# Kernel optimization log

Measured on AMD Instinct MI355X. Metric: run time of the kernel, lower is better.

The kernel has to match this reference:

```python
import jax, jax.numpy as jnp
import numpy as np

N, E, G, B = 50000, 1600000, 128, 128
FP = 33     # num_feature_pro
ED = 128    # embed_dim
ML = 3000   # max_len


def setup_inputs() -> dict:
    key = jax.random.key(0)
    ks = jax.random.split(key, 20)
    s = lambda k, shape: jax.random.normal(k, shape, jnp.float32) * 0.02
    inp = {}
    inp["pro_x"] = jax.random.normal(ks[0], (N, FP), jnp.float32)
    inp["edge_index"] = jax.random.randint(ks[1], (2, E), 0, N)
    inp["edge_weight"] = jax.random.uniform(ks[2], (E,), jnp.float32)
    inp["pro_batch"] = jnp.sort(jax.random.randint(ks[3], (N,), 0, G))
    inp["rna_global"] = jax.random.randint(ks[4], (B, ML), 0, 5)
    inp["rna_local"] = jax.random.randint(ks[5], (B, ML - 2), 0, 65)
    inp["emb1"] = s(ks[6], (5, ED))
    inp["emb2"] = s(ks[7], (65, ED))
    inp["convW1"] = s(ks[8], (32, ML, 8));     inp["convb1"] = jnp.zeros((32,), jnp.float32)
    inp["convW2"] = s(ks[9], (32, ML - 2, 8)); inp["convb2"] = jnp.zeros((32,), jnp.float32)
    inp["fcxr_W"] = s(ks[10], (32 * 121, 128)); inp["fcxr_b"] = jnp.zeros((128,), jnp.float32)
    inp["gcn1_W"] = s(ks[11], (FP, FP));         inp["gcn1_b"] = jnp.zeros((FP,), jnp.float32)
    inp["gcn2_W"] = s(ks[12], (FP, 2 * FP));     inp["gcn2_b"] = jnp.zeros((2 * FP,), jnp.float32)
    inp["gcn3_W"] = s(ks[13], (2 * FP, 4 * FP)); inp["gcn3_b"] = jnp.zeros((4 * FP,), jnp.float32)
    inp["bn1_g"] = jnp.ones((FP,), jnp.float32);     inp["bn1_b"] = jnp.zeros((FP,), jnp.float32)
    inp["bn2_g"] = jnp.ones((2 * FP,), jnp.float32); inp["bn2_b"] = jnp.zeros((2 * FP,), jnp.float32)
    inp["bn3_g"] = jnp.ones((4 * FP,), jnp.float32); inp["bn3_b"] = jnp.zeros((4 * FP,), jnp.float32)
    inp["fcg1_W"] = s(ks[14], (4 * FP, 1024)); inp["fcg1_b"] = jnp.zeros((1024,), jnp.float32)
    inp["fcg2_W"] = s(ks[15], (1024, 128));    inp["fcg2_b"] = jnp.zeros((128,), jnp.float32)
    return inp


def _gcn(x, W, b, src, dst, ew, n):
    # PyG GCNConv: x' = D^{-1/2}(A+I)D^{-1/2} (x W) + b, self-loop weight 1
    xw = x @ W                                           # [n, out]
    deg = jax.ops.segment_sum(ew, dst, num_segments=n) + 1.0
    dis = jax.lax.rsqrt(deg)
    norm = dis[src] * ew * dis[dst]                      # [E]
    out = jax.ops.segment_sum(xw[src] * norm[:, None], dst, num_segments=n)
    out = out + xw * (dis * dis)[:, None]                # self loops
    return out + b


def _bn(x, g, b, eps=1e-5):
    # NodeLevelBatchNorm (training): batch stats over the node dim, biased var
    m = x.mean(0)
    v = ((x - m) ** 2).mean(0)
    return (x - m) * jax.lax.rsqrt(v + eps) * g + b


def _conv1d(x, W, b):
    # x: [B, C, L], W: [O, C, K] -> [B, O, L-K+1]
    y = jax.lax.conv_general_dilated(x, W, (1,), 'VALID',
                                     dimension_numbers=('NCH', 'OIH', 'NCH'))
    return y + b[None, :, None]


def _rna(tok, emb, cW, cb, fW, fb):
    e = emb[tok]                     # [B, seq, 128] -> channels=seq, length=128
    y = _conv1d(e, cW, cb)           # [B, 32, 121]
    return y.reshape(y.shape[0], -1) @ fW + fb


def reference(pro_x, edge_index, edge_weight, pro_batch, rna_global, rna_local,
              emb1, emb2, convW1, convb1, convW2, convb2, fcxr_W, fcxr_b,
              gcn1_W, gcn1_b, gcn2_W, gcn2_b, gcn3_W, gcn3_b,
              bn1_g, bn1_b, bn2_g, bn2_b, bn3_g, bn3_b,
              fcg1_W, fcg1_b, fcg2_W, fcg2_b):
    src, dst = edge_index[0], edge_index[1]
    n = pro_x.shape[0]
    # RNA branch (fc_xr shared between global and local)
    xrg = _rna(rna_global, emb1, convW1, convb1, fcxr_W, fcxr_b)
    xrl = _rna(rna_local, emb2, convW2, convb2, fcxr_W, fcxr_b)
    # Protein GCN branch
    xp = jax.nn.relu(_bn(_gcn(pro_x, gcn1_W, gcn1_b, src, dst, edge_weight, n), bn1_g, bn1_b))
    ones = jnp.ones_like(edge_weight)
    xp = jax.nn.relu(_bn(_gcn(xp, gcn2_W, gcn2_b, src, dst, ones, n), bn2_g, bn2_b))
    xp = jax.nn.relu(_bn(_gcn(xp, gcn3_W, gcn3_b, src, dst, ones, n), bn3_g, bn3_b))
    # global mean pool per graph
    cnt = jax.ops.segment_sum(jnp.ones((n,), xp.dtype), pro_batch, num_segments=G)
    pooled = jax.ops.segment_sum(xp, pro_batch, num_segments=G) / jnp.maximum(cnt, 1.0)[:, None]
    h = jax.nn.relu(pooled @ fcg1_W + fcg1_b)
    xp_out = h @ fcg2_W + fcg2_b     # dropout = identity (eval)
    xc_rna = (xrg + xrl) * 0.5       # mean over stacked [xrg, xrl]
    return (xc_rna, xp_out)
```

## Files before the change

kernel.cpp:

```cpp
#include <hip/hip_runtime.h>
#include <hip/hip_bf16.h>

typedef __hip_bfloat16 bf16;
typedef unsigned short u16;

#define NN 50000
#define NE 1600000
#define NG 128
#define NB 128
#define SG 3000
#define SL 2998
#define VG 5
#define VL 65
#define EDB 6250
#define AGB 12500
#define NA  (NB*VG + NB*VL)
#define NGB (32*VG + 32*VL)
#define CASTB ((NN*40+255)/256)
#define NSTR 8

__device__ __forceinline__ float b2f(bf16 x){ return __bfloat162float(x); }
__device__ __forceinline__ float blo(unsigned u){ return __uint_as_float(u << 16); }
__device__ __forceinline__ float bhi(unsigned u){ return __uint_as_float(u & 0xffff0000u); }

__global__ void k_front(const int* __restrict__ rna_g, const int* __restrict__ rna_l,
                        int* __restrict__ tcnt_g, int* __restrict__ toff_g,
                        u16* __restrict__ bucket_g,
                        int* __restrict__ tcnt_l, int* __restrict__ toff_l,
                        u16* __restrict__ bucket_l,
                        const float* __restrict__ convW1, const float* __restrict__ convW2,
                        float* __restrict__ Wr1, float* __restrict__ Wr2,
                        const float* __restrict__ fcxrW, const float* __restrict__ cb1,
                        const float* __restrict__ cb2, float* __restrict__ bias0,
                        const int* __restrict__ dst, const float* __restrict__ ew,
                        double* __restrict__ packed, int* __restrict__ slot){
    int bx = blockIdx.x;
    int t = threadIdx.x;
    if (bx < 2*NB){
        __shared__ int hist[VL], pre[VL], cur[VL];
        int br = bx & 1, b = bx >> 1;
        const int* tok = br ? rna_l : rna_g;
        int S = br ? SL : SG, V = br ? VL : VG;
        int* tcnt = br ? tcnt_l : tcnt_g;
        int* toff = br ? toff_l : toff_g;
        u16* bucket = br ? bucket_l : bucket_g;
        if (t < V) hist[t] = 0;
        __syncthreads();
        for (int i = t; i < S; i += 256) atomicAdd(&hist[tok[b*S + i]], 1);
        __syncthreads();
        if (t == 0){
            int run = 0;
            for (int v = 0; v < V; ++v){ pre[v] = run; run += hist[v]; }
        }
        __syncthreads();
        if (t < V){
            tcnt[b*V + t] = hist[t];
            toff[b*V + t] = pre[t];
            cur[t] = pre[t];
        }
        __syncthreads();
        for (int i = t; i < S; i += 256){
            int v = tok[b*S + i];
            int p = atomicAdd(&cur[v], 1);
            bucket[b*S + p] = (u16)i;
        }
        return;
    }
    bx -= 2*NB;
    if (bx < EDB){
        int e = bx*256 + t;
        double old = unsafeAtomicAdd(&packed[dst[e]], 1048576.0 + (double)ew[e]);
        slot[e] = (int)(old * (1.0/1048576.0));
        return;
    }
    bx -= EDB;
    if (bx < SG + SL){
        const float* W; float* Wr; int S, c = bx;
        if (c < SG){ W = convW1; Wr = Wr1; S = SG; }
        else { c -= SG; W = convW2; Wr = Wr2; S = SL; }
        Wr[c*256 + t] = W[((t >> 3)*S + c)*8 + (t & 7)];
        return;
    }
    bx -= SG + SL;
    if (t >= 128) return;
    int o = bx, j = t;
    float s = 0.f;
    const float* Wo = fcxrW + o*121*128 + j;
    for (int l = 0; l < 121; ++l) s += Wo[l*128];
    unsafeAtomicAdd(&bias0[j], 0.5f * (cb1[o] + cb2[o]) * s);
}

__device__ void dev_buildA(const float* __restrict__ Wr, const u16* __restrict__ bucket,
                           const int* __restrict__ toff, const int* __restrict__ tcnt,
                           float* __restrict__ A, int S, int V, int bv){
    int b = bv / V, v = bv - b*V;
    int t = threadIdx.x;
    const u16* bk = bucket + b*S + toff[b*V + v];
    int m = tcnt[b*V + v];
    float acc = 0.f;
    int idx = 0;
    for (; idx + 4 <= m; idx += 4){
        int c0 = bk[idx], c1 = bk[idx+1], c2 = bk[idx+2], c3 = bk[idx+3];
        acc += Wr[c0*256 + t];
        acc += Wr[c1*256 + t];
        acc += Wr[c2*256 + t];
        acc += Wr[c3*256 + t];
    }
    for (; idx < m; ++idx) acc += Wr[bk[idx]*256 + t];
    A[b*(256*V) + v*256 + t] = acc;
}

__global__ void k_F1(const float* __restrict__ Wr1, const float* __restrict__ Wr2,
                     const u16* __restrict__ bucket_g, const int* __restrict__ toff_g,
                     const int* __restrict__ tcnt_g, float* __restrict__ Ag,
                     const u16* __restrict__ bucket_l, const int* __restrict__ toff_l,
                     const int* __restrict__ tcnt_l, float* __restrict__ Al,
                     const double* __restrict__ packed, int* __restrict__ cnt,
                     float2* __restrict__ dis12, float2* __restrict__ self12,
                     const int* __restrict__ batch, int* __restrict__ gstart,
                     int* __restrict__ bsum,
                     const float* __restrict__ fcxrb, const float* __restrict__ bias0,
                     float* __restrict__ out0){
    __shared__ int sd[256];
    int bx = blockIdx.x;
    if (bx < NA){
        if (bx < NB*VG) dev_buildA(Wr1, bucket_g, toff_g, tcnt_g, Ag, SG, VG, bx);
        else dev_buildA(Wr2, bucket_l, toff_l, tcnt_l, Al, SL, VL, bx - NB*VG);
        return;
    }
    bx -= NA;
    int t = threadIdx.x;
    if (bx == 49){
        for (int idx = t; idx < NB*128; idx += 256)
            out0[idx] = fcxrb[idx & 127] + bias0[idx & 127];
        return;
    }
    int base = bx*1024;
    int s = 0;
    #pragma unroll
    for (int j = 0; j < 4; ++j){
        int i = base + t*4 + j;
        if (i < NN){
            double p = packed[i];
            int c = (int)(p * (1.0/1048576.0));
            float w = (float)(p - (double)c * 1048576.0);
            cnt[i] = c; s += c;
            float r1 = rsqrtf(w + 1.0f);
            float r2 = rsqrtf((float)c + 1.0f);
            dis12[i] = make_float2(r1, r2);
            self12[i] = make_float2(r1*r1, r2*r2);
            int pb = batch[i];
            int prev = (i == 0) ? -1 : batch[i-1];
            for (int g = prev + 1; g <= pb; ++g) gstart[g] = i;
            if (i == NN - 1){
                for (int g = pb + 1; g <= NG; ++g) gstart[g] = NN;
            }
        }
    }
    sd[t] = s; __syncthreads();
    for (int d = 128; d > 0; d >>= 1){
        if (t < d) sd[t] += sd[t+d];
        __syncthreads();
    }
    if (t == 0) bsum[bx] = sd[0];
}

__global__ void k_scan3(const int* __restrict__ cnt, const int* __restrict__ bsum,
                        int* __restrict__ offs){
    __shared__ int sd[256];
    __shared__ int sbase;
    int t = threadIdx.x;
    if (t == 0){
        int run = 0;
        for (int i = 0; i < blockIdx.x; ++i) run += bsum[i];
        sbase = run;
    }
    int base = blockIdx.x*1024;
    int loc[4]; int s = 0;
    #pragma unroll
    for (int j = 0; j < 4; ++j){
        int idx = base + t*4 + j;
        loc[j] = (idx < NN) ? cnt[idx] : 0;
        s += loc[j];
    }
    sd[t] = s; __syncthreads();
    for (int d = 1; d < 256; d <<= 1){
        int v = (t >= d) ? sd[t-d] : 0;
        __syncthreads();
        sd[t] += v;
        __syncthreads();
    }
    int run = sbase + (sd[t] - s);
    #pragma unroll
    for (int j = 0; j < 4; ++j){
        int idx = base + t*4 + j;
        if (idx < NN) offs[idx] = run;
        run += loc[j];
    }
}

__device__ void dev_buildG(float (*rows)[128], const float* __restrict__ emb,
                           const float* __restrict__ W, bf16* __restrict__ G,
                           int V, int q){
    int o = q / V, mt = q - o*V;
    int t = threadIdx.x;
    int j = t & 127, half = t >> 7;
    int kk[4], vv[4];
    #pragma unroll
    for (int qq = 0; qq < 4; ++qq){
        int mm = half*4 + qq;
        int m = mt*8 + mm;
        int k = m / V, v = m - k*V;
        kk[qq] = k; vv[qq] = v;
        rows[mm][j] = emb[v*128 + j];
    }
    __syncthreads();
    float a0=0.f, a1=0.f, a2=0.f, a3=0.f;
    const float* Wo = W + o*121*128 + j;
    for (int l = 0; l < 121; ++l){
        float w = Wo[l*128];
        a0 += rows[half*4+0][l + kk[0]] * w;
        a1 += rows[half*4+1][l + kk[1]] * w;
        a2 += rows[half*4+2][l + kk[2]] * w;
        a3 += rows[half*4+3][l + kk[3]] * w;
    }
    float a[4] = {a0, a1, a2, a3};
    #pragma unroll
    for (int qq = 0; qq < 4; ++qq){
        int row = vv[qq]*256 + o*8 + kk[qq];
        G[(size_t)row*128 + j] = __float2bfloat16(a[qq]);
    }
}

__global__ void k_F2(const int* __restrict__ src, const int* __restrict__ dst,
                     const float* __restrict__ ew, const float2* __restrict__ dis12,
                     const int* __restrict__ offs, const int* __restrict__ slot,
                     float4* __restrict__ epk,
                     const float* __restrict__ emb1, const float* __restrict__ emb2,
                     const float* __restrict__ fcxrW, bf16* __restrict__ G1,
                     bf16* __restrict__ G2,
                     const float* __restrict__ pro_x, bf16* __restrict__ xb0){
    __shared__ float rows[8][128];
    int bx = blockIdx.x;
    if (bx < 32*VG){ dev_buildG(rows, emb1, fcxrW, G1, VG, bx); return; }
    if (bx < NGB){ dev_buildG(rows, emb2, fcxrW, G2, VL, bx - 32*VG); return; }
    bx -= NGB;
    if (bx < EDB){
        int e = bx*256 + threadIdx.x;
        int s = src[e], d = dst[e];
        int pos = offs[d] + slot[e];
        float2 a = dis12[s], b = dis12[d];
        float4 v;
        v.x = __int_as_float(s*80);
        v.y = a.x * ew[e] * b.x;
        v.z = a.y * b.y;
        v.w = __int_as_float(s*144);
        epk[pos] = v;
        return;
    }
    bx -= EDB;
    int i = bx*256 + threadIdx.x;
    if (i >= NN*40) return;
    int n = i / 40, f = i - n*40;
    xb0[i] = __float2bfloat16(f < 33 ? pro_x[n*33 + f] : 0.f);
}

template<int QV, int GRP, int OFF_W, int N_Z>
__device__ void dev_agg(float* sAgg ,
                        const bf16* __restrict__ xb, const float4* __restrict__ epk,
                        const int* __restrict__ offs, const int* __restrict__ cnt,
                        const float2* __restrict__ self12,
                        const float* __restrict__ W, const float* __restrict__ bias,
                        float* __restrict__ tout, float* __restrict__ bnpart,
                        int F, int OF, int bx){
    const int LPG = 64 / GRP;
    int wave = threadIdx.x >> 6;
    int node = bx*4 + wave;
    int lane = threadIdx.x & 63;
    int grp  = lane / LPG;
    int gl   = lane % LPG;
    bool act = gl < QV;
    const char* xc = (const char*)xb;
    float a0=0,a1=0,a2=0,a3=0,a4=0,a5=0,a6=0,a7=0;
    int b = offs[node], e = b + cnt[node];
    if (act){
        int fo = gl << 4;
        if (grp == 0){
            float2 sw2 = self12[node];
            float sw = N_Z ? sw2.y : sw2.x;
            uint4 u = *(const uint4*)(xc + node*(QV*16) + fo);
            a0 = sw*blo(u.x); a1 = sw*bhi(u.x); a2 = sw*blo(u.y); a3 = sw*bhi(u.y);
            a4 = sw*blo(u.z); a5 = sw*bhi(u.z); a6 = sw*blo(u.w); a7 = sw*bhi(u.w);
        }
        int p = b + grp;
        for (; p + 3*GRP < e; p += 4*GRP){
            float4 e0 = epk[p];
            float4 e1 = epk[p +   GRP];
            float4 e2 = epk[p + 2*GRP];
            float4 e3 = epk[p + 3*GRP];
            int o0 = __float_as_int(OFF_W ? e0.w : e0.x); float n0 = N_Z ? e0.z : e0.y;
            int o1 = __float_as_int(OFF_W ? e1.w : e1.x); float n1 = N_Z ? e1.z : e1.y;
            int o2 = __float_as_int(OFF_W ? e2.w : e2.x); float n2 = N_Z ? e2.z : e2.y;
            int o3 = __float_as_int(OFF_W ? e3.w : e3.x); float n3 = N_Z ? e3.z : e3.y;
            uint4 u0 = *(const uint4*)(xc + o0 + fo);
            uint4 u1 = *(const uint4*)(xc + o1 + fo);
            uint4 u2 = *(const uint4*)(xc + o2 + fo);
            uint4 u3 = *(const uint4*)(xc + o3 + fo);
            a0 += n0*blo(u0.x); a1 += n0*bhi(u0.x); a2 += n0*blo(u0.y); a3 += n0*bhi(u0.y);
            a4 += n0*blo(u0.z); a5 += n0*bhi(u0.z); a6 += n0*blo(u0.w); a7 += n0*bhi(u0.w);
            a0 += n1*blo(u1.x); a1 += n1*bhi(u1.x); a2 += n1*blo(u1.y); a3 += n1*bhi(u1.y);
            a4 += n1*blo(u1.z); a5 += n1*bhi(u1.z); a6 += n1*blo(u1.w); a7 += n1*bhi(u1.w);
            a0 += n2*blo(u2.x); a1 += n2*bhi(u2.x); a2 += n2*blo(u2.y); a3 += n2*bhi(u2.y);
            a4 += n2*blo(u2.z); a5 += n2*bhi(u2.z); a6 += n2*blo(u2.w); a7 += n2*bhi(u2.w);
            a0 += n3*blo(u3.x); a1 += n3*bhi(u3.x); a2 += n3*blo(u3.y); a3 += n3*bhi(u3.y);
            a4 += n3*blo(u3.z); a5 += n3*bhi(u3.z); a6 += n3*blo(u3.w); a7 += n3*bhi(u3.w);
        }
        if (p < e){
            int p1 = p + GRP, p2 = p + 2*GRP;
            bool v1 = p1 < e, v2 = p2 < e;
            float4 e0 = epk[p];
            float4 e1 = epk[v1 ? p1 : p];
            float4 e2 = epk[v2 ? p2 : p];
            int o0 = __float_as_int(OFF_W ? e0.w : e0.x);
            int o1 = __float_as_int(OFF_W ? e1.w : e1.x);
            int o2 = __float_as_int(OFF_W ? e2.w : e2.x);
            float n0 = N_Z ? e0.z : e0.y;
            float n1 = v1 ? (N_Z ? e1.z : e1.y) : 0.f;
            float n2 = v2 ? (N_Z ? e2.z : e2.y) : 0.f;
            uint4 u0 = *(const uint4*)(xc + o0 + fo);
            uint4 u1 = *(const uint4*)(xc + o1 + fo);
            uint4 u2 = *(const uint4*)(xc + o2 + fo);
            a0 += n0*blo(u0.x); a1 += n0*bhi(u0.x); a2 += n0*blo(u0.y); a3 += n0*bhi(u0.y);
            a4 += n0*blo(u0.z); a5 += n0*bhi(u0.z); a6 += n0*blo(u0.w); a7 += n0*bhi(u0.w);
            a0 += n1*blo(u1.x); a1 += n1*bhi(u1.x); a2 += n1*blo(u1.y); a3 += n1*bhi(u1.y);
            a4 += n1*blo(u1.z); a5 += n1*bhi(u1.z); a6 += n1*blo(u1.w); a7 += n1*bhi(u1.w);
            a0 += n2*blo(u2.x); a1 += n2*bhi(u2.x); a2 += n2*blo(u2.y); a3 += n2*bhi(u2.y);
            a4 += n2*blo(u2.z); a5 += n2*bhi(u2.z); a6 += n2*blo(u2.w); a7 += n2*bhi(u2.w);
        }
    }
    #pragma unroll
    for (int m = LPG; m < 64; m <<= 1){
        a0 += __shfl_xor(a0, m); a1 += __shfl_xor(a1, m);
        a2 += __shfl_xor(a2, m); a3 += __shfl_xor(a3, m);
        a4 += __shfl_xor(a4, m); a5 += __shfl_xor(a5, m);
        a6 += __shfl_xor(a6, m); a7 += __shfl_xor(a7, m);
    }
    if (act && grp == 0){
        float4* dst = (float4*)&sAgg[wave*(QV*8) + gl*8];
        dst[0] = make_float4(a0, a1, a2, a3);
        dst[1] = make_float4(a4, a5, a6, a7);
    }
    __syncthreads();
    int i0 = bx*4;
    int j = threadIdx.x;
    if (j < OF){
        float c0 = bias[j], c1 = c0, c2 = c0, c3 = c0;
        const float* Wj = W + j;
        const float* s0 = sAgg;
        const float* s1 = sAgg + QV*8;
        const float* s2 = sAgg + 2*QV*8;
        const float* s3 = sAgg + 3*QV*8;
        #pragma unroll 4
        for (int f = 0; f < F; ++f){
            float w = Wj[f*OF];
            c0 += s0[f]*w; c1 += s1[f]*w; c2 += s2[f]*w; c3 += s3[f]*w;
        }
        tout[(size_t)(i0+0)*OF + j] = c0;
        tout[(size_t)(i0+1)*OF + j] = c1;
        tout[(size_t)(i0+2)*OF + j] = c2;
        tout[(size_t)(i0+3)*OF + j] = c3;
        float s  = c0 + c1 + c2 + c3;
        float ss = c0*c0 + c1*c1 + c2*c2 + c3*c3;
        float* part = bnpart + (bx & (NSTR-1))*(2*OF);
        unsafeAtomicAdd(&part[j], s);
        unsafeAtomicAdd(&part[OF + j], ss);
    }
}

template<int QV, int GRP, int OFF_W, int N_Z>
__global__ __launch_bounds__(256, 8)
void k_agg_gemm(const bf16* __restrict__ xb, const float4* __restrict__ epk,
                const int* __restrict__ offs, const int* __restrict__ cnt,
                const float2* __restrict__ self12,
                const float* __restrict__ W, const float* __restrict__ bias,
                float* __restrict__ tout, float* __restrict__ bnpart,
                int F, int OF){
    __shared__ float sAgg[4*QV*8];
    dev_agg<QV,GRP,OFF_W,N_Z>(sAgg, xb, epk, offs, cnt, self12, W, bias,
                              tout, bnpart, F, OF, blockIdx.x);
}

__device__ void dev_gemmR(float* xs , int bq,
                          const float* __restrict__ Ag, const bf16* __restrict__ G1,
                          const float* __restrict__ Al, const bf16* __restrict__ G2,
                          float* __restrict__ out0){
    int kpart = bq >> 4;
    int bgrp  = bq & 15;
    const float* X; const bf16* G; int K, k0;
    if (kpart < 5){ X = Ag; G = G1; K = 1280;  k0 = kpart*256; }
    else          { X = Al; G = G2; K = 16640; k0 = (kpart-5)*256; }
    int b0 = bgrp*8;
    int t = threadIdx.x;
    #pragma unroll
    for (int i = 0; i < 8; ++i)
        xs[i*256 + t] = X[(b0+i)*K + k0 + t];
    __syncthreads();
    int rq = t >> 7, j = t & 127;
    const float* x0 = xs + (rq*4)*256;
    float a0=0,a1=0,a2=0,a3=0;
    const bf16* Gp = G + (size_t)k0*128 + j;
    for (int kk = 0; kk < 256; ++kk){
        float g = b2f(Gp[kk*128]);
        a0 += x0[kk]*g; a1 += x0[256+kk]*g; a2 += x0[512+kk]*g; a3 += x0[768+kk]*g;
    }
    unsafeAtomicAdd(&out0[(b0+rq*4+0)*128 + j], 0.5f*a0);
    unsafeAtomicAdd(&out0[(b0+rq*4+1)*128 + j], 0.5f*a1);
    unsafeAtomicAdd(&out0[(b0+rq*4+2)*128 + j], 0.5f*a2);
    unsafeAtomicAdd(&out0[(b0+rq*4+3)*128 + j], 0.5f*a3);
}

__global__ void k_L3(const bf16* __restrict__ xb, const float4* __restrict__ epk,
                     const int* __restrict__ offs, const int* __restrict__ cnt,
                     const float2* __restrict__ self12,
                     const float* __restrict__ W, const float* __restrict__ bias,
                     float* __restrict__ tout, float* __restrict__ bnpart,
                     const float* __restrict__ Ag, const bf16* __restrict__ G1,
                     const float* __restrict__ Al, const bf16* __restrict__ G2,
                     float* __restrict__ out0){
    __shared__ float smem[8*256];
    int bx = blockIdx.x;
    if (bx < AGB){
        dev_agg<9,4,1,1>(smem, xb, epk, offs, cnt, self12, W, bias, tout, bnpart,
                         66, 132, bx);
    } else {
        dev_gemmR(smem, bx - AGB, Ag, G1, Al, G2, out0);
    }
}

__global__ void k_bn_apply(const float* __restrict__ t, const float* __restrict__ part,
                           const float* __restrict__ g, const float* __restrict__ b,
                           bf16* __restrict__ xo, int OF, int OS, int total){
    __shared__ float fs[264];
    int tid = threadIdx.x;
    for (int i = tid; i < 2*OF; i += 256){
        float s = 0.f;
        #pragma unroll
        for (int k = 0; k < NSTR; ++k) s += part[k*(2*OF) + i];
        fs[i] = s;
    }
    __syncthreads();
    int id = blockIdx.x*256 + tid;
    if (id >= total) return;
    int i = id / OS, f = id - i*OS;
    float v = 0.f;
    if (f < OF){
        float m  = fs[f] * (1.0f/(float)NN);
        float vr = fs[OF + f] * (1.0f/(float)NN) - m*m;
        float sc = g[f] * rsqrtf(vr + 1e-5f);
        float sh = b[f] - m*sc;
        v = t[(size_t)i*OF + f] * sc + sh;
        v = v > 0.f ? v : 0.f;
    }
    xo[id] = __float2bfloat16(v);
}

__global__ void k_fcgF(const float* __restrict__ bufB, const float* __restrict__ part3,
                       const float* __restrict__ bn3g, const float* __restrict__ bn3b,
                       const int* __restrict__ gstart,
                       const float* __restrict__ W1, const float* __restrict__ b1,
                       const float* __restrict__ W2, const float* __restrict__ b2,
                       float* __restrict__ out){
    __shared__ float fs[264];
    __shared__ float scs[132], shs[132];
    __shared__ float pp[7][132];
    __shared__ float pr[132];
    __shared__ float hr[1024];
    __shared__ float part[8][128];
    int g = blockIdx.x, t = threadIdx.x;
    for (int i = t; i < 264; i += 1024){
        float s = 0.f;
        #pragma unroll
        for (int k = 0; k < NSTR; ++k) s += part3[k*264 + i];
        fs[i] = s;
    }
    __syncthreads();
    if (t < 132){
        float m  = fs[t] * (1.0f/(float)NN);
        float vr = fs[132 + t] * (1.0f/(float)NN) - m*m;
        float sc = bn3g[t] * rsqrtf(vr + 1e-5f);
        scs[t] = sc;
        shs[t] = bn3b[t] - m*sc;
    }
    __syncthreads();
    int i0 = gstart[g], i1 = gstart[g+1];
    int r = t / 132, f = t - r*132;
    if (r < 7){
        float acc = 0.f;
        for (int i = i0 + r; i < i1; i += 7){
            float v = bufB[(size_t)i*132 + f] * scs[f] + shs[f];
            acc += v > 0.f ? v : 0.f;
        }
        pp[r][f] = acc;
    }
    __syncthreads();
    if (t < 132){
        float s = 0.f;
        #pragma unroll
        for (int k = 0; k < 7; ++k) s += pp[k][t];
        float inv = 1.0f / fmaxf((float)(i1 - i0), 1.0f);
        pr[t] = s * inv;
    }
    __syncthreads();
    float acc = b1[t];
    #pragma unroll 4
    for (int ff = 0; ff < 132; ++ff) acc += pr[ff] * W1[ff*1024 + t];
    hr[t] = acc > 0.f ? acc : 0.f;
    __syncthreads();
    int ks = t >> 7, j = t & 127;
    const float* Wp = W2 + (ks*128)*128 + j;
    const float* hp = hr + ks*128;
    float a = 0.f;
    #pragma unroll 8
    for (int kk = 0; kk < 128; ++kk) a += hp[kk] * Wp[(size_t)kk*128];
    part[ks][j] = a;
    __syncthreads();
    if (t < 128){
        float s = b2[t];
        #pragma unroll
        for (int rr = 0; rr < 8; ++rr) s += part[rr][t];
        out[g*128 + t] = s;
    }
}

extern "C" void kernel_launch(void* const* d_in, const int* in_sizes, int n_in,
                              void* d_out, int out_size, void* d_ws, size_t ws_size,
                              hipStream_t stream)
{
    (void)in_sizes; (void)n_in; (void)out_size; (void)ws_size;

    const float* pro_x  = (const float*)d_in[0];
    const int*   eidx   = (const int*)  d_in[1];
    const float* ew     = (const float*)d_in[2];
    const int*   pbatch = (const int*)  d_in[3];
    const int*   rna_g  = (const int*)  d_in[4];
    const int*   rna_l  = (const int*)  d_in[5];
    const float* emb1   = (const float*)d_in[6];
    const float* emb2   = (const float*)d_in[7];
    const float* convW1 = (const float*)d_in[8];
    const float* convb1 = (const float*)d_in[9];
    const float* convW2 = (const float*)d_in[10];
    const float* convb2 = (const float*)d_in[11];
    const float* fcxrW  = (const float*)d_in[12];
    const float* fcxrb  = (const float*)d_in[13];
    const float* g1W = (const float*)d_in[14];
    const float* g1b = (const float*)d_in[15];
    const float* g2W = (const float*)d_in[16];
    const float* g2b = (const float*)d_in[17];
    const float* g3W = (const float*)d_in[18];
    const float* g3b = (const float*)d_in[19];
    const float* bn1g = (const float*)d_in[20];
    const float* bn1b = (const float*)d_in[21];
    const float* bn2g = (const float*)d_in[22];
    const float* bn2b = (const float*)d_in[23];
    const float* bn3g = (const float*)d_in[24];
    const float* bn3b = (const float*)d_in[25];
    const float* fcg1W = (const float*)d_in[26];
    const float* fcg1b = (const float*)d_in[27];
    const float* fcg2W = (const float*)d_in[28];
    const float* fcg2b = (const float*)d_in[29];

    const int* e_src = eidx;
    const int* e_dst = eidx + NE;

    char* base = (char*)d_ws;
    size_t off = 0;
    auto alloc = [&](size_t bytes)->char*{
        off = (off + 255) & ~(size_t)255;
        char* p = base + off; off += bytes; return p;
    };

    double* packed  = (double*)alloc(NN*8);
    float* bias0   = (float*)alloc(128*4);
    float* bnpart1 = (float*)alloc(NSTR*2*33*4);
    float* bnpart2 = (float*)alloc(NSTR*2*66*4);
    float* bnpart3 = (float*)alloc(NSTR*2*132*4);
    size_t zero_bytes = (off + 255) & ~(size_t)255;

    int*    cnt    = (int*)   alloc(NN*4);
    float2* dis12  = (float2*)alloc(NN*8);
    float2* self12 = (float2*)alloc(NN*8);
    int*    offs   = (int*)   alloc(NN*4);
    int*    bsum   = (int*)   alloc(64*4);
    int*    gstart = (int*)   alloc((NG+1)*4);
    float4* epk    = (float4*)alloc((size_t)NE*16);
    float*  bufB   = (float*) alloc((size_t)NN*132*4);
    bf16*   xbA    = (bf16*)  alloc((size_t)NE*4);
    bf16*   xbB    = (bf16*)  alloc((size_t)NN*72*2);
    float*  Ag     = (float*) alloc((size_t)NB*256*VG*4);
    float*  Al     = (float*) alloc((size_t)NB*256*VL*4);
    bf16*   G1     = (bf16*)  alloc((size_t)32*8*VG*128*2);
    bf16*   G2     = (bf16*)  alloc((size_t)32*8*VL*128*2);

    int*  slot = (int*)xbA;
    bf16* xb0  = (bf16*)xbB;

    float* out0 = (float*)d_out;
    float* out1 = (float*)d_out + 16384;

    char* rb = (char*)bufB;
    size_t ro = 0;
    auto ralloc = [&](size_t bytes)->char*{
        ro = (ro + 255) & ~(size_t)255;
        char* p = rb + ro; ro += bytes; return p;
    };
    int* toff_g   = (int*)ralloc(NB*VG*4);
    int* toff_l   = (int*)ralloc(NB*VL*4);
    int* tcnt_g   = (int*)ralloc(NB*VG*4);
    int* tcnt_l   = (int*)ralloc(NB*VL*4);
    u16* bucket_g = (u16*)ralloc((size_t)NB*SG*2);
    u16* bucket_l = (u16*)ralloc((size_t)NB*SL*2);
    float* Wr1    = (float*)ralloc((size_t)SG*256*4);
    float* Wr2    = (float*)ralloc((size_t)SL*256*4);

    hipMemsetAsync(d_ws, 0, zero_bytes, stream);

    k_front<<<2*NB + EDB + SG + SL + 32, 256, 0, stream>>>(
        rna_g, rna_l, tcnt_g, toff_g, bucket_g, tcnt_l, toff_l, bucket_l,
        convW1, convW2, Wr1, Wr2, fcxrW, convb1, convb2, bias0,
        e_dst, ew, packed, slot);

    k_F1<<<NA + 50, 256, 0, stream>>>(Wr1, Wr2,
                                      bucket_g, toff_g, tcnt_g, Ag,
                                      bucket_l, toff_l, tcnt_l, Al,
                                      packed, cnt, dis12, self12, pbatch, gstart,
                                      bsum, fcxrb, bias0, out0);
    k_scan3<<<49, 256, 0, stream>>>(cnt, bsum, offs);

    k_F2<<<NGB + EDB + CASTB, 256, 0, stream>>>(
        e_src, e_dst, ew, dis12, offs, slot, epk,
        emb1, emb2, fcxrW, G1, G2, pro_x, xb0);

    k_agg_gemm<5,8,0,0><<<AGB, 256, 0, stream>>>(xb0, epk, offs, cnt, self12,
                                                 g1W, g1b, bufB, bnpart1, 33, 33);
    k_bn_apply<<<(NN*40+255)/256, 256, 0, stream>>>(bufB, bnpart1, bn1g, bn1b,
                                                    xbA, 33, 40, NN*40);

    k_agg_gemm<5,8,0,1><<<AGB, 256, 0, stream>>>(xbA, epk, offs, cnt, self12,
                                                 g2W, g2b, bufB, bnpart2, 33, 66);
    k_bn_apply<<<(NN*72+255)/256, 256, 0, stream>>>(bufB, bnpart2, bn2g, bn2b,
                                                    xbB, 66, 72, NN*72);

    k_L3<<<AGB + 1120, 256, 0, stream>>>(xbB, epk, offs, cnt, self12,
                                         g3W, g3b, bufB, bnpart3, Ag, G1, Al, G2, out0);

    k_fcgF<<<NG, 1024, 0, stream>>>(bufB, bnpart3, bn3g, bn3b, gstart,
                                    fcg1W, fcg1b, fcg2W, fcg2b, out1);
}
```

Measured before the change: 656.7 us.

## Spread BN atomics over 64 stripes, reduce them in a separate kernel, prefetch edges

Raises the number of striped partial-sum buffers for batch-norm statistics from 8 to 64 to cut atomic contention in the aggregation kernels. A new single-block kernel reduces the 64 stripes once into a sums buffer, so the apply and final kernels no longer redo the reduction in every block. It also software-pipelines the edge-record loads in the aggregation loop, fetching the next group of four while the current group is processed. The cost is three extra kernel launches, a larger zeroed workspace, and more live registers in the aggregation loop.

Result: faster. 580.6 us (-11.6%).

```diff
diff --git a/kernel.cpp b/kernel.cpp
--- a/kernel.cpp
+++ b/kernel.cpp
@@ -17,7 +17,6 @@
 #define NA  (NB*VG + NB*VL)
 #define NGB (32*VG + 32*VL)
 #define CASTB ((NN*40+255)/256)
-#define NSTR 8
 
 __device__ __forceinline__ float b2f(bf16 x){ return __bfloat162float(x); }
 __device__ __forceinline__ float blo(unsigned u){ return __uint_as_float(u << 16); }
@@ -283,6 +282,7 @@
     const char* xc = (const char*)xb;
     float a0=0,a1=0,a2=0,a3=0,a4=0,a5=0,a6=0,a7=0;
     int b = offs[node], e = b + cnt[node];
+    int p = b + grp;
     if (act){
         int fo = gl << 4;
         if (grp == 0){
@@ -292,28 +292,41 @@
             a0 = sw*blo(u.x); a1 = sw*bhi(u.x); a2 = sw*blo(u.y); a3 = sw*bhi(u.y);
             a4 = sw*blo(u.z); a5 = sw*bhi(u.z); a6 = sw*blo(u.w); a7 = sw*bhi(u.w);
         }
-        int p = b + grp;
-        for (; p + 3*GRP < e; p += 4*GRP){
+        if (p + 3*GRP < e){
             float4 e0 = epk[p];
             float4 e1 = epk[p +   GRP];
             float4 e2 = epk[p + 2*GRP];
             float4 e3 = epk[p + 3*GRP];
-            int o0 = __float_as_int(OFF_W ? e0.w : e0.x); float n0 = N_Z ? e0.z : e0.y;
-            int o1 = __float_as_int(OFF_W ? e1.w : e1.x); float n1 = N_Z ? e1.z : e1.y;
-            int o2 = __float_as_int(OFF_W ? e2.w : e2.x); float n2 = N_Z ? e2.z : e2.y;
-            int o3 = __float_as_int(OFF_W ? e3.w : e3.x); float n3 = N_Z ? e3.z : e3.y;
-            uint4 u0 = *(const uint4*)(xc + o0 + fo);
-            uint4 u1 = *(const uint4*)(xc + o1 + fo);
-            uint4 u2 = *(const uint4*)(xc + o2 + fo);
-            uint4 u3 = *(const uint4*)(xc + o3 + fo);
-            a0 += n0*blo(u0.x); a1 += n0*bhi(u0.x); a2 += n0*blo(u0.y); a3 += n0*bhi(u0.y);
-            a4 += n0*blo(u0.z); a5 += n0*bhi(u0.z); a6 += n0*blo(u0.w); a7 += n0*bhi(u0.w);
-            a0 += n1*blo(u1.x); a1 += n1*bhi(u1.x); a2 += n1*blo(u1.y); a3 += n1*bhi(u1.y);
-            a4 += n1*blo(u1.z); a5 += n1*bhi(u1.z); a6 += n1*blo(u1.w); a7 += n1*bhi(u1.w);
-            a0 += n2*blo(u2.x); a1 += n2*bhi(u2.x); a2 += n2*blo(u2.y); a3 += n2*bhi(u2.y);
-            a4 += n2*blo(u2.z); a5 += n2*bhi(u2.z); a6 += n2*blo(u2.w); a7 += n2*bhi(u2.w);
-            a0 += n3*blo(u3.x); a1 += n3*bhi(u3.x); a2 += n3*blo(u3.y); a3 += n3*bhi(u3.y);
-            a4 += n3*blo(u3.z); a5 += n3*bhi(u3.z); a6 += n3*blo(u3.w); a7 += n3*bhi(u3.w);
+            for (;;){
+                int pn = p + 4*GRP;
+                bool more = pn + 3*GRP < e;
+                float4 f0, f1, f2, f3;
+                if (more){
+                    f0 = epk[pn];
+                    f1 = epk[pn +   GRP];
+                    f2 = epk[pn + 2*GRP];
+                    f3 = epk[pn + 3*GRP];
+                }
+                int o0 = __float_as_int(OFF_W ? e0.w : e0.x); float n0 = N_Z ? e0.z : e0.y;
+                int o1 = __float_as_int(OFF_W ? e1.w : e1.x); float n1 = N_Z ? e1.z : e1.y;
+                int o2 = __float_as_int(OFF_W ? e2.w : e2.x); float n2 = N_Z ? e2.z : e2.y;
+                int o3 = __float_as_int(OFF_W ? e3.w : e3.x); float n3 = N_Z ? e3.z : e3.y;
+                uint4 u0 = *(const uint4*)(xc + o0 + fo);
+                uint4 u1 = *(const uint4*)(xc + o1 + fo);
+                uint4 u2 = *(const uint4*)(xc + o2 + fo);
+                uint4 u3 = *(const uint4*)(xc + o3 + fo);
+                a0 += n0*blo(u0.x); a1 += n0*bhi(u0.x); a2 += n0*blo(u0.y); a3 += n0*bhi(u0.y);
+                a4 += n0*blo(u0.z); a5 += n0*bhi(u0.z); a6 += n0*blo(u0.w); a7 += n0*bhi(u0.w);
+                a0 += n1*blo(u1.x); a1 += n1*bhi(u1.x); a2 += n1*blo(u1.y); a3 += n1*bhi(u1.y);
+                a4 += n1*blo(u1.z); a5 += n1*bhi(u1.z); a6 += n1*blo(u1.w); a7 += n1*bhi(u1.w);
+                a0 += n2*blo(u2.x); a1 += n2*bhi(u2.x); a2 += n2*blo(u2.y); a3 += n2*bhi(u2.y);
+                a4 += n2*blo(u2.z); a5 += n2*bhi(u2.z); a6 += n2*blo(u2.w); a7 += n2*bhi(u2.w);
+                a0 += n3*blo(u3.x); a1 += n3*bhi(u3.x); a2 += n3*blo(u3.y); a3 += n3*bhi(u3.y);
+                a4 += n3*blo(u3.z); a5 += n3*bhi(u3.z); a6 += n3*blo(u3.w); a7 += n3*bhi(u3.w);
+                p = pn;
+                if (!more) break;
+                e0 = f0; e1 = f1; e2 = f2; e3 = f3;
+            }
         }
         if (p < e){
             int p1 = p + GRP, p2 = p + 2*GRP;
@@ -371,7 +384,7 @@
         tout[(size_t)(i0+3)*OF + j] = c3;
         float s  = c0 + c1 + c2 + c3;
         float ss = c0*c0 + c1*c1 + c2*c2 + c3*c3;
-        float* part = bnpart + (bx & (NSTR-1))*(2*OF);
+        float* part = bnpart + (bx & 63)*(2*OF);
         unsafeAtomicAdd(&part[j], s);
         unsafeAtomicAdd(&part[OF + j], ss);
     }
@@ -437,25 +450,25 @@
     }
 }
 
-__global__ void k_bn_apply(const float* __restrict__ t, const float* __restrict__ part,
+__global__ void k_bn_fin(const float* __restrict__ part, float* __restrict__ sums, int OF){
+    int tid = threadIdx.x;
+    if (tid >= 2*OF) return;
+    float s = 0.f;
+    #pragma unroll 8
+    for (int k = 0; k < 64; ++k) s += part[k*(2*OF) + tid];
+    sums[tid] = s;
+}
+
+__global__ void k_bn_apply(const float* __restrict__ t, const float* __restrict__ sums,
                            const float* __restrict__ g, const float* __restrict__ b,
                            bf16* __restrict__ xo, int OF, int OS, int total){
-    __shared__ float fs[264];
-    int tid = threadIdx.x;
-    for (int i = tid; i < 2*OF; i += 256){
-        float s = 0.f;
-        #pragma unroll
-        for (int k = 0; k < NSTR; ++k) s += part[k*(2*OF) + i];
-        fs[i] = s;
-    }
-    __syncthreads();
-    int id = blockIdx.x*256 + tid;
+    int id = blockIdx.x*256 + threadIdx.x;
     if (id >= total) return;
     int i = id / OS, f = id - i*OS;
     float v = 0.f;
     if (f < OF){
-        float m  = fs[f] * (1.0f/(float)NN);
-        float vr = fs[OF + f] * (1.0f/(float)NN) - m*m;
+        float m  = sums[f] * (1.0f/(float)NN);
+        float vr = sums[OF + f] * (1.0f/(float)NN) - m*m;
         float sc = g[f] * rsqrtf(vr + 1e-5f);
         float sh = b[f] - m*sc;
         v = t[(size_t)i*OF + f] * sc + sh;
@@ -464,29 +477,21 @@
     xo[id] = __float2bfloat16(v);
 }
 
-__global__ void k_fcgF(const float* __restrict__ bufB, const float* __restrict__ part3,
+__global__ void k_fcgF(const float* __restrict__ bufB, const float* __restrict__ sums,
                        const float* __restrict__ bn3g, const float* __restrict__ bn3b,
                        const int* __restrict__ gstart,
                        const float* __restrict__ W1, const float* __restrict__ b1,
                        const float* __restrict__ W2, const float* __restrict__ b2,
                        float* __restrict__ out){
-    __shared__ float fs[264];
     __shared__ float scs[132], shs[132];
     __shared__ float pp[7][132];
     __shared__ float pr[132];
     __shared__ float hr[1024];
     __shared__ float part[8][128];
     int g = blockIdx.x, t = threadIdx.x;
-    for (int i = t; i < 264; i += 1024){
-        float s = 0.f;
-        #pragma unroll
-        for (int k = 0; k < NSTR; ++k) s += part3[k*264 + i];
-        fs[i] = s;
-    }
-    __syncthreads();
     if (t < 132){
-        float m  = fs[t] * (1.0f/(float)NN);
-        float vr = fs[132 + t] * (1.0f/(float)NN) - m*m;
+        float m  = sums[t] * (1.0f/(float)NN);
+        float vr = sums[132 + t] * (1.0f/(float)NN) - m*m;
         float sc = bn3g[t] * rsqrtf(vr + 1e-5f);
         scs[t] = sc;
         shs[t] = bn3b[t] - m*sc;
@@ -580,10 +585,13 @@
     };
 
     double* packed  = (double*)alloc(NN*8);
+    float* bnsum1  = (float*)alloc(2*33*4);
+    float* bnsum2  = (float*)alloc(2*66*4);
+    float* bnsum3  = (float*)alloc(2*132*4);
     float* bias0   = (float*)alloc(128*4);
-    float* bnpart1 = (float*)alloc(NSTR*2*33*4);
-    float* bnpart2 = (float*)alloc(NSTR*2*66*4);
-    float* bnpart3 = (float*)alloc(NSTR*2*132*4);
+    float* bnpart1 = (float*)alloc(64*2*33*4);
+    float* bnpart2 = (float*)alloc(64*2*66*4);
+    float* bnpart3 = (float*)alloc(64*2*132*4);
     size_t zero_bytes = (off + 255) & ~(size_t)255;
 
     int*    cnt    = (int*)   alloc(NN*4);
@@ -642,17 +650,20 @@
 
     k_agg_gemm<5,8,0,0><<<AGB, 256, 0, stream>>>(xb0, epk, offs, cnt, self12,
                                                  g1W, g1b, bufB, bnpart1, 33, 33);
-    k_bn_apply<<<(NN*40+255)/256, 256, 0, stream>>>(bufB, bnpart1, bn1g, bn1b,
+    k_bn_fin<<<1, 512, 0, stream>>>(bnpart1, bnsum1, 33);
+    k_bn_apply<<<(NN*40+255)/256, 256, 0, stream>>>(bufB, bnsum1, bn1g, bn1b,
                                                     xbA, 33, 40, NN*40);
 
     k_agg_gemm<5,8,0,1><<<AGB, 256, 0, stream>>>(xbA, epk, offs, cnt, self12,
                                                  g2W, g2b, bufB, bnpart2, 33, 66);
-    k_bn_apply<<<(NN*72+255)/256, 256, 0, stream>>>(bufB, bnpart2, bn2g, bn2b,
+    k_bn_fin<<<1, 512, 0, stream>>>(bnpart2, bnsum2, 66);
+    k_bn_apply<<<(NN*72+255)/256, 256, 0, stream>>>(bufB, bnsum2, bn2g, bn2b,
                                                     xbB, 66, 72, NN*72);
 
     k_L3<<<AGB + 1120, 256, 0, stream>>>(xbB, epk, offs, cnt, self12,
                                          g3W, g3b, bufB, bnpart3, Ag, G1, Al, G2, out0);
-
-    k_fcgF<<<NG, 1024, 0, stream>>>(bufB, bnpart3, bn3g, bn3b, gstart,
+    k_bn_fin<<<1, 512, 0, stream>>>(bnpart3, bnsum3, 132);
+
+    k_fcgF<<<NG, 1024, 0, stream>>>(bufB, bnsum3, bn3g, bn3b, gstart,
                                     fcg1W, fcg1b, fcg2W, fcg2b, out1);
 }
```
